# Optimization experiments

Hardware: AMD Instinct MI355X
Metric: run time of the kernel (lower is better)

## Reference

```python
import jax, jax.numpy as jnp
import numpy as np

N_NODES = 50000
N_EDGES = 800000
D = 64


def setup_inputs() -> dict:
    key = jax.random.key(0)
    k1, k2, k3, k4, k5, k6, k7 = jax.random.split(key, 7)
    h = jax.random.normal(k1, (N_NODES, D), dtype=jnp.float32)
    x = jax.random.normal(k2, (N_NODES, 3), dtype=jnp.float32)
    edge_index = jax.random.randint(k3, (2, N_EDGES), 0, N_NODES, dtype=jnp.int64)
    # fc_h: Linear(D, D); fc_x: Linear(D, 1). PyTorch default init scale ~1/sqrt(fan_in).
    s = 1.0 / np.sqrt(D)
    W_h = jax.random.uniform(k4, (D, D), minval=-s, maxval=s, dtype=jnp.float32)
    b_h = jax.random.uniform(k5, (D,), minval=-s, maxval=s, dtype=jnp.float32)
    W_x = jax.random.uniform(k6, (D, 1), minval=-s, maxval=s, dtype=jnp.float32)
    b_x = jax.random.uniform(k7, (1,), minval=-s, maxval=s, dtype=jnp.float32)
    return {"h": h, "x": x, "edge_index": edge_index,
            "W_h": W_h, "b_h": b_h, "W_x": W_x, "b_x": b_x}


def reference(h, x, edge_index, W_h, b_h, W_x, b_x):
    row, col = edge_index[0], edge_index[1]
    h_j = h[col]                                   # [E, D] gather
    delta_x = x[row] - x[col]                      # [E, 3]
    m = jax.nn.relu(h_j @ W_h + b_h)               # [E, D]
    agg_h = jax.ops.segment_sum(m, row, num_segments=h.shape[0])
    h_new = h + agg_h
    weight = jax.nn.relu(h_j @ W_x + b_x)          # [E, 1]
    agg_x = jax.ops.segment_sum(delta_x * weight, row, num_segments=x.shape[0])
    x_new = x + agg_x
    return (h_new, x_new)
```

## Files before the change

kernel.cpp:

```cpp
#include <hip/hip_runtime.h>
#include <hip/hip_fp16.h>

#define N_NODES 50000
#define N_EDGES 800000
#define D 64
#define BLOCK 256

#define NBIN 256
#define BINW 196
#define BCAP 3584
#define EPB 4096
#define NBINBLK 196
#define PREBLK 196
#define SUBS 4
#define RNODES 49
#define QCAP 1024

__global__ __launch_bounds__(BLOCK) void pre_bin_kernel(
    const float* __restrict__ h, const float* __restrict__ x,
    const int* __restrict__ eidx,
    const float* __restrict__ Wh, const float* __restrict__ bh,
    const float* __restrict__ Wx, const float* __restrict__ bx,
    __half2* __restrict__ M16, float4* __restrict__ px,
    int* __restrict__ bins, int* __restrict__ gcur) {
  const unsigned b = blockIdx.x;

  if (b < NBINBLK) {
    __shared__ int cnt[NBIN], ssc[NBIN], start[NBIN], cur[NBIN], gbase[NBIN];
    __shared__ int stage[EPB];
    const int t = threadIdx.x;
    cnt[t] = 0;
    __syncthreads();
    const int base = (int)b * EPB;
#pragma unroll 4
    for (int k = 0; k < EPB / BLOCK; ++k) {
      int e = base + k * BLOCK + t;
      if (e < N_EDGES) {
        int row = eidx[e];
        if ((unsigned)row < N_NODES) atomicAdd(&cnt[row / BINW], 1);
      }
    }
    __syncthreads();
    ssc[t] = cnt[t];
    __syncthreads();
    for (int off = 1; off < NBIN; off <<= 1) {
      int v = (t >= off) ? ssc[t - off] : 0;
      __syncthreads();
      ssc[t] += v;
      __syncthreads();
    }
    int ex = ssc[t] - cnt[t];
    start[t] = ex;
    cur[t] = ex;
    gbase[t] = cnt[t] ? atomicAdd(&gcur[t], cnt[t]) : 0;
    __syncthreads();
#pragma unroll 4
    for (int k = 0; k < EPB / BLOCK; ++k) {
      int e = base + k * BLOCK + t;
      if (e < N_EDGES) {
        int row = eidx[e];
        int col = eidx[N_EDGES + e];
        if ((unsigned)row < N_NODES && (unsigned)col < N_NODES) {
          int bb = row / BINW;
          int pos = atomicAdd(&cur[bb], 1);
          stage[pos] = (bb << 24) | ((row - bb * BINW) << 16) | col;
        }
      }
    }
    __syncthreads();
    const int total = ssc[NBIN - 1];
    for (int idx = t; idx < total; idx += BLOCK) {
      int e = stage[idx];
      int bb = ((unsigned)e) >> 24;
      int dst = gbase[bb] + (idx - start[bb]);
      if (dst < BCAP) bins[(size_t)bb * BCAP + dst] = e;
    }
    return;
  }

  const int pid = (int)b - NBINBLK;
  const int i = pid * BLOCK + threadIdx.x;
  if (i >= N_NODES) return;

  const float4* __restrict__ h4 = (const float4*)(h + (size_t)i * D);
  const float4* __restrict__ Wx4 = (const float4*)Wx;

  float acc[D];
#pragma unroll
  for (int d = 0; d < D; ++d) acc[d] = bh[d];
  float wx = bx[0];

  for (int q = 0; q < D / 4; ++q) {
    float4 hv = h4[q];
    float4 wxv = Wx4[q];
    wx = fmaf(hv.x, wxv.x, fmaf(hv.y, wxv.y, fmaf(hv.z, wxv.z,
         fmaf(hv.w, wxv.w, wx))));
#pragma unroll
    for (int r = 0; r < 4; ++r) {
      float hk = (r == 0) ? hv.x : (r == 1) ? hv.y : (r == 2) ? hv.z : hv.w;
      const float4* wr4 = (const float4*)(Wh + (q * 4 + r) * D);
#pragma unroll
      for (int dq = 0; dq < D / 4; ++dq) {
        float4 wv = wr4[dq];
        acc[4 * dq + 0] = fmaf(hk, wv.x, acc[4 * dq + 0]);
        acc[4 * dq + 1] = fmaf(hk, wv.y, acc[4 * dq + 1]);
        acc[4 * dq + 2] = fmaf(hk, wv.z, acc[4 * dq + 2]);
        acc[4 * dq + 3] = fmaf(hk, wv.w, acc[4 * dq + 3]);
      }
    }
  }

  __half2 hh[D / 2];
#pragma unroll
  for (int j = 0; j < D / 2; ++j)
    hh[j] = __floats2half2_rn(fmaxf(acc[2 * j], 0.0f),
                              fmaxf(acc[2 * j + 1], 0.0f));
  float4* mrow = (float4*)(M16 + (size_t)i * 32);
  const float4* hhp = (const float4*)hh;
#pragma unroll
  for (int q = 0; q < 8; ++q) mrow[q] = hhp[q];

  float w = fmaxf(wx, 0.0f);
  px[i] = make_float4(w, w * x[(size_t)i * 3 + 0],
                      w * x[(size_t)i * 3 + 1],
                      w * x[(size_t)i * 3 + 2]);
}

__global__ __launch_bounds__(256) void agg_kernel(
    const float* __restrict__ h, const float* __restrict__ x,
    const int* __restrict__ bins, const int* __restrict__ gcur,
    const __half2* __restrict__ M16, const float4* __restrict__ px,
    float* __restrict__ out) {
  __shared__ int qs[QCAP];
  __shared__ int hist[RNODES];
  __shared__ int rstart[RNODES + 1];
  __shared__ int rcur[RNODES];

  const int t = threadIdx.x;
  const int bin = blockIdx.x >> 2, sub = blockIdx.x & 3;
  const int lbase = sub * RNODES;
  const int gb = bin * BINW + lbase;
  const int R = min(RNODES, N_NODES - gb);
  if (R <= 0) return;

  if (t < RNODES) hist[t] = 0;
  __syncthreads();

  const int n = min(gcur[bin], BCAP);
  const int* bs = bins + (size_t)bin * BCAP;
  for (int i = t; i < n; i += 256) {
    int e = bs[i];
    unsigned dd = (unsigned)((e >> 16) & 0xff) - (unsigned)lbase;
    if (dd < (unsigned)R) atomicAdd(&hist[dd], 1);
  }
  __syncthreads();
  if (t < 64) {
    int myh = (t < R) ? hist[t] : 0;
    int v = myh;
#pragma unroll
    for (int off = 1; off < 64; off <<= 1) {
      int u = __shfl_up(v, off);
      if (t >= off) v += u;
    }
    if (t == 0) rstart[0] = 0;
    if (t < R) { rstart[t + 1] = v; rcur[t] = v - myh; }
  }
  __syncthreads();
  for (int i = t; i < n; i += 256) {
    int e = bs[i];
    unsigned dd = (unsigned)((e >> 16) & 0xff) - (unsigned)lbase;
    if (dd < (unsigned)R) {
      int pos = atomicAdd(&rcur[dd], 1);
      if (pos < QCAP) qs[pos] = e;
    }
  }
  __syncthreads();

  const float* pxf = (const float*)px;
  const float2* M2 = (const float2*)M16;
  const int l16 = t & 15;
  const int stream = t >> 4;
  const int wbase = t & 48;
  const size_t xb = (size_t)N_NODES * D;

  for (int rr = stream; rr < R; rr += 16) {
    int beg = min(rstart[rr], QCAP);
    int end = min(rstart[rr + 1], QCAP);
    float a0 = 0.f, a1 = 0.f, a2 = 0.f, a3 = 0.f, ps = 0.f;
    for (int qi = beg; qi < end; qi += 8) {
      float2 g[8];
      float pv[8];
      bool val[8];
#pragma unroll
      for (int j = 0; j < 8; ++j) {
        int idx = qi + j;
        val[j] = idx < end;
        int e = qs[val[j] ? idx : beg];
        int c = e & 0xffff;
        pv[j] = 0.f;
        if (val[j]) {
          g[j] = M2[(size_t)c * 16 + l16];
          if (l16 < 4) pv[j] = pxf[c * 4 + l16];
        }
      }
#pragma unroll
      for (int j = 0; j < 8; ++j)
        if (val[j]) {
          const __half2* hp = (const __half2*)&g[j];
          float2 f0 = __half22float2(hp[0]);
          float2 f1 = __half22float2(hp[1]);
          a0 += f0.x; a1 += f0.y; a2 += f1.x; a3 += f1.y;
          ps += pv[j];
        }
    }
    int gn = gb + rr;
    float4 hvv = ((const float4*)h)[(size_t)gn * 16 + l16];
    ((float4*)out)[(size_t)gn * 16 + l16] =
        make_float4(hvv.x + a0, hvv.y + a1, hvv.z + a2, hvv.w + a3);
    float W = __shfl(ps, wbase);
    float pc = __shfl(ps, wbase + l16 + 1);
    if (l16 < 3)
      out[xb + (size_t)gn * 3 + l16] =
          fmaf(x[(size_t)gn * 3 + l16], 1.0f + W, -pc);
  }
}


__global__ __launch_bounds__(256) void init_out_kernel(
    const float* __restrict__ h, const float* __restrict__ x,
    float* __restrict__ out) {
  const int NH4 = N_NODES * D / 4;
  const int NT4 = (N_NODES * D + N_NODES * 3) / 4;
  int i = blockIdx.x * 256 + threadIdx.x;
  if (i >= NT4) return;
  float4 v;
  if (i < NH4) v = ((const float4*)h)[i];
  else         v = ((const float4*)x)[i - NH4];
  ((float4*)out)[i] = v;
}

__global__ __launch_bounds__(256) void edge_kernel(
    const float* __restrict__ h, const float* __restrict__ x,
    const int* __restrict__ eidx,
    const float* __restrict__ Wh, const float* __restrict__ bh,
    const float* __restrict__ Wx, const float* __restrict__ bx,
    float* __restrict__ out) {
  int e = blockIdx.x * 256 + threadIdx.x;
  if (e >= N_EDGES) return;
  int row = eidx[e];
  int col = eidx[N_EDGES + e];
  if ((unsigned)row >= N_NODES || (unsigned)col >= N_NODES) return;
  const float* hj = h + (size_t)col * D;
  float acc[D];
#pragma unroll
  for (int dd = 0; dd < D; ++dd) acc[dd] = bh[dd];
  float wsum = bx[0];
#pragma unroll 2
  for (int kg = 0; kg < D / 4; ++kg) {
    float4 hv = *(const float4*)(hj + kg * 4);
#pragma unroll
    for (int j = 0; j < 4; ++j) {
      float hk = (j == 0) ? hv.x : (j == 1) ? hv.y : (j == 2) ? hv.z : hv.w;
      int k = kg * 4 + j;
      wsum = fmaf(hk, Wx[k], wsum);
      const float* wrow = Wh + k * D;
#pragma unroll
      for (int dd = 0; dd < D; ++dd) acc[dd] = fmaf(hk, wrow[dd], acc[dd]);
    }
  }
  float* outh = out + (size_t)row * D;
#pragma unroll
  for (int dd = 0; dd < D; ++dd) atomicAdd(&outh[dd], fmaxf(acc[dd], 0.0f));
  float w = fmaxf(wsum, 0.0f);
  float* outx = out + (size_t)N_NODES * D + (size_t)row * 3;
  const float* xr = x + (size_t)row * 3;
  const float* xc = x + (size_t)col * 3;
#pragma unroll
  for (int c = 0; c < 3; ++c) atomicAdd(&outx[c], (xr[c] - xc[c]) * w);
}


extern "C" void kernel_launch(void* const* d_in, const int* in_sizes, int n_in,
                              void* d_out, int out_size, void* d_ws, size_t ws_size,
                              hipStream_t stream) {
  const float* h    = (const float*)d_in[0];
  const float* x    = (const float*)d_in[1];
  const int*   eidx = (const int*)d_in[2];
  const float* Wh   = (const float*)d_in[3];
  const float* bh   = (const float*)d_in[4];
  const float* Wx   = (const float*)d_in[5];
  const float* bx   = (const float*)d_in[6];
  float* out = (float*)d_out;

  size_t need = (size_t)N_NODES * D * 2 + (size_t)N_NODES * 16 +
                (size_t)NBIN * BCAP * 4 + 1024;

  if (ws_size < need) {
    const int NT4 = (N_NODES * D + N_NODES * 3) / 4;
    init_out_kernel<<<(NT4 + 255) / 256, 256, 0, stream>>>(h, x, out);
    edge_kernel<<<(N_EDGES + 255) / 256, 256, 0, stream>>>(
        h, x, eidx, Wh, bh, Wx, bx, out);
    return;
  }

  __half2* M16 = (__half2*)d_ws;
  float4*  px  = (float4*)((char*)d_ws + (size_t)N_NODES * D * 2);
  int*     bins = (int*)((char*)px + (size_t)N_NODES * 16);
  int*     gcur = bins + (size_t)NBIN * BCAP;

  hipMemsetAsync(gcur, 0, NBIN * sizeof(int), stream);
  pre_bin_kernel<<<NBINBLK + PREBLK, BLOCK, 0, stream>>>(
      h, x, eidx, Wh, bh, Wx, bx, M16, px, bins, gcur);
  agg_kernel<<<NBIN * SUBS, 256, 0, stream>>>(
      h, x, bins, gcur, M16, px, out);
}
```

Measured before the change: 128.6 us.

## Fuse binning, node transform and aggregation into one cooperative kernel

Merges the pre-bin/node-transform kernel and the aggregation kernel into a single cooperative launch of 512 blocks separated by a grid-wide sync. Each block both bins a slice of edges and computes M16/px for 98 nodes, then aggregates half a bin, staging the bin's entries in LDS before the two passes. The aim is to remove one kernel launch boundary and spread work over more blocks. The cost is a grid barrier, larger LDS use that may limit residency, and only 98 of 256 threads doing the dense node transform, with the old two-kernel path kept as a fallback if the cooperative launch fails.

```diff
diff --git a/kernel.cpp b/kernel.cpp
--- a/kernel.cpp
+++ b/kernel.cpp
@@ -1,20 +1,247 @@
 #include <hip/hip_runtime.h>
 #include <hip/hip_fp16.h>
+#include <hip/hip_cooperative_groups.h>
+
+namespace cg = cooperative_groups;
 
 #define N_NODES 50000
 #define N_EDGES 800000
 #define D 64
 #define BLOCK 256
+#define GRID 512
 
 #define NBIN 256
 #define BINW 196
 #define BCAP 3584
+#define EPBF 1563
+#define KITF 7
+#define STAGEB 1568
+#define RNODES 98
+#define QCAP 1920
+
 #define EPB 4096
 #define NBINBLK 196
 #define PREBLK 196
-#define SUBS 4
-#define RNODES 49
-#define QCAP 1024
+#define SUBS_F 4
+#define RN_F 49
+#define QCAP_F 1024
+
+__global__ __launch_bounds__(BLOCK) void fused_kernel(
+    const float* __restrict__ h, const float* __restrict__ x,
+    const int* __restrict__ eidx,
+    const float* __restrict__ Wh, const float* __restrict__ bh,
+    const float* __restrict__ Wx, const float* __restrict__ bx,
+    __half2* __restrict__ M16, float4* __restrict__ px,
+    int* __restrict__ bins, int* __restrict__ gcur,
+    float* __restrict__ out) {
+  __shared__ union {
+    struct {
+      int cnt[NBIN], ssc[NBIN], start[NBIN], cur[NBIN], gbase[NBIN];
+      int stage[STAGEB];
+    } bl;
+    struct {
+      int stage2[BCAP];
+      int qs[QCAP];
+      int sc[128];
+      int hist[RNODES], rcur[RNODES];
+      int rstart[RNODES + 1];
+    } ag;
+  } S;
+
+  const int b = blockIdx.x;
+  const int t = threadIdx.x;
+
+  S.bl.cnt[t] = 0;
+  __syncthreads();
+  const int ebase = b * EPBF;
+  const int eend = min(ebase + EPBF, N_EDGES);
+#pragma unroll
+  for (int k = 0; k < KITF; ++k) {
+    int e = ebase + k * BLOCK + t;
+    if (e < eend) {
+      int row = eidx[e];
+      if ((unsigned)row < N_NODES) atomicAdd(&S.bl.cnt[row / BINW], 1);
+    }
+  }
+  __syncthreads();
+  S.bl.ssc[t] = S.bl.cnt[t];
+  __syncthreads();
+  for (int off = 1; off < NBIN; off <<= 1) {
+    int v = (t >= off) ? S.bl.ssc[t - off] : 0;
+    __syncthreads();
+    S.bl.ssc[t] += v;
+    __syncthreads();
+  }
+  {
+    int ex = S.bl.ssc[t] - S.bl.cnt[t];
+    S.bl.start[t] = ex;
+    S.bl.cur[t] = ex;
+    S.bl.gbase[t] = S.bl.cnt[t] ? atomicAdd(&gcur[t], S.bl.cnt[t]) : 0;
+  }
+  __syncthreads();
+#pragma unroll
+  for (int k = 0; k < KITF; ++k) {
+    int e = ebase + k * BLOCK + t;
+    if (e < eend) {
+      int row = eidx[e];
+      int col = eidx[N_EDGES + e];
+      if ((unsigned)row < N_NODES && (unsigned)col < N_NODES) {
+        int bb = row / BINW;
+        int pos = atomicAdd(&S.bl.cur[bb], 1);
+        S.bl.stage[pos] = (bb << 24) | ((row - bb * BINW) << 16) | col;
+      }
+    }
+  }
+  __syncthreads();
+  {
+    const int total = S.bl.ssc[NBIN - 1];
+    for (int idx = t; idx < total; idx += BLOCK) {
+      int e = S.bl.stage[idx];
+      int bb = ((unsigned)e) >> 24;
+      int dst = S.bl.gbase[bb] + (idx - S.bl.start[bb]);
+      if (dst < BCAP) bins[(size_t)bb * BCAP + dst] = e;
+    }
+  }
+
+  {
+    const int i = b * RNODES + t;
+    if (t < RNODES && i < N_NODES) {
+      const float4* __restrict__ h4 = (const float4*)(h + (size_t)i * D);
+      const float4* __restrict__ Wx4 = (const float4*)Wx;
+      float acc[D];
+#pragma unroll
+      for (int d = 0; d < D; ++d) acc[d] = bh[d];
+      float wx = bx[0];
+      for (int q = 0; q < D / 4; ++q) {
+        float4 hv = h4[q];
+        float4 wxv = Wx4[q];
+        wx = fmaf(hv.x, wxv.x, fmaf(hv.y, wxv.y,
+             fmaf(hv.z, wxv.z, fmaf(hv.w, wxv.w, wx))));
+#pragma unroll
+        for (int r = 0; r < 4; ++r) {
+          float hk = (r == 0) ? hv.x : (r == 1) ? hv.y : (r == 2) ? hv.z : hv.w;
+          const float4* wr4 = (const float4*)(Wh + (q * 4 + r) * D);
+#pragma unroll
+          for (int dq = 0; dq < D / 4; ++dq) {
+            float4 wv = wr4[dq];
+            acc[4 * dq + 0] = fmaf(hk, wv.x, acc[4 * dq + 0]);
+            acc[4 * dq + 1] = fmaf(hk, wv.y, acc[4 * dq + 1]);
+            acc[4 * dq + 2] = fmaf(hk, wv.z, acc[4 * dq + 2]);
+            acc[4 * dq + 3] = fmaf(hk, wv.w, acc[4 * dq + 3]);
+          }
+        }
+      }
+      __half2 hh[D / 2];
+#pragma unroll
+      for (int j = 0; j < D / 2; ++j)
+        hh[j] = __floats2half2_rn(fmaxf(acc[2 * j], 0.0f),
+                                  fmaxf(acc[2 * j + 1], 0.0f));
+      float4* mrow = (float4*)(M16 + (size_t)i * 32);
+      const float4* hhp = (const float4*)hh;
+#pragma unroll
+      for (int q = 0; q < 8; ++q) mrow[q] = hhp[q];
+      float w = fmaxf(wx, 0.0f);
+      px[i] = make_float4(w, w * x[(size_t)i * 3 + 0],
+                          w * x[(size_t)i * 3 + 1],
+                          w * x[(size_t)i * 3 + 2]);
+    }
+  }
+
+  __threadfence();
+  cg::this_grid().sync();
+  __threadfence();
+
+  {
+    const int bin = b >> 1, sub = b & 1;
+    const int lbase = sub * RNODES;
+    const int gb = bin * BINW + lbase;
+    const int R = min(RNODES, N_NODES - gb);
+    if (R > 0) {
+      if (t < RNODES) S.ag.hist[t] = 0;
+      __syncthreads();
+      const int n = min(gcur[bin], BCAP);
+      const int* bs = bins + (size_t)bin * BCAP;
+      for (int ii = t; ii < n; ii += BLOCK) {
+        int e = bs[ii];
+        S.ag.stage2[ii] = e;
+        unsigned dd = (unsigned)((e >> 16) & 0xff) - (unsigned)lbase;
+        if (dd < (unsigned)R) atomicAdd(&S.ag.hist[dd], 1);
+      }
+      __syncthreads();
+      if (t < 128) S.ag.sc[t] = (t < R) ? S.ag.hist[t] : 0;
+      __syncthreads();
+      for (int off = 1; off < 128; off <<= 1) {
+        int v = (t < 128 && t >= off) ? S.ag.sc[t - off] : 0;
+        __syncthreads();
+        if (t < 128) S.ag.sc[t] += v;
+        __syncthreads();
+      }
+      if (t == 0) S.ag.rstart[0] = 0;
+      if (t < R) {
+        S.ag.rstart[t + 1] = S.ag.sc[t];
+        S.ag.rcur[t] = S.ag.sc[t] - S.ag.hist[t];
+      }
+      __syncthreads();
+      for (int ii = t; ii < n; ii += BLOCK) {
+        int e = S.ag.stage2[ii];
+        unsigned dd = (unsigned)((e >> 16) & 0xff) - (unsigned)lbase;
+        if (dd < (unsigned)R) {
+          int pos = atomicAdd(&S.ag.rcur[dd], 1);
+          if (pos < QCAP) S.ag.qs[pos] = e;
+        }
+      }
+      __syncthreads();
+
+      const float* pxf = (const float*)px;
+      const float2* M2 = (const float2*)M16;
+      const int l16 = t & 15;
+      const int stream = t >> 4;
+      const int wbase = t & 48;
+      const size_t xb = (size_t)N_NODES * D;
+
+      for (int rr = stream; rr < R; rr += 16) {
+        int beg = min(S.ag.rstart[rr], QCAP);
+        int end = min(S.ag.rstart[rr + 1], QCAP);
+        float a0 = 0.f, a1 = 0.f, a2 = 0.f, a3 = 0.f, ps = 0.f;
+        for (int qi = beg; qi < end; qi += 8) {
+          float2 g[8];
+          float pv[8];
+          bool val[8];
+#pragma unroll
+          for (int j = 0; j < 8; ++j) {
+            int idx = qi + j;
+            val[j] = idx < end;
+            int e = S.ag.qs[val[j] ? idx : beg];
+            int c = e & 0xffff;
+            pv[j] = 0.f;
+            if (val[j]) {
+              g[j] = M2[(size_t)c * 16 + l16];
+              if (l16 < 4) pv[j] = pxf[c * 4 + l16];
+            }
+          }
+#pragma unroll
+          for (int j = 0; j < 8; ++j)
+            if (val[j]) {
+              const __half2* hp = (const __half2*)&g[j];
+              float2 f0 = __half22float2(hp[0]);
+              float2 f1 = __half22float2(hp[1]);
+              a0 += f0.x; a1 += f0.y; a2 += f1.x; a3 += f1.y;
+              ps += pv[j];
+            }
+        }
+        int gn = gb + rr;
+        float4 hvv = ((const float4*)h)[(size_t)gn * 16 + l16];
+        ((float4*)out)[(size_t)gn * 16 + l16] =
+            make_float4(hvv.x + a0, hvv.y + a1, hvv.z + a2, hvv.w + a3);
+        float W = __shfl(ps, wbase);
+        float pc = __shfl(ps, wbase + l16 + 1);
+        if (l16 < 3)
+          out[xb + (size_t)gn * 3 + l16] =
+              fmaf(x[(size_t)gn * 3 + l16], 1.0f + W, -pc);
+      }
+    }
+  }
+}
 
 __global__ __launch_bounds__(BLOCK) void pre_bin_kernel(
     const float* __restrict__ h, const float* __restrict__ x,
@@ -24,7 +251,6 @@
     __half2* __restrict__ M16, float4* __restrict__ px,
     int* __restrict__ bins, int* __restrict__ gcur) {
   const unsigned b = blockIdx.x;
-
   if (b < NBINBLK) {
     __shared__ int cnt[NBIN], ssc[NBIN], start[NBIN], cur[NBIN], gbase[NBIN];
     __shared__ int stage[EPB];
@@ -50,8 +276,7 @@
       __syncthreads();
     }
     int ex = ssc[t] - cnt[t];
-    start[t] = ex;
-    cur[t] = ex;
+    start[t] = ex; cur[t] = ex;
     gbase[t] = cnt[t] ? atomicAdd(&gcur[t], cnt[t]) : 0;
     __syncthreads();
 #pragma unroll 4
@@ -77,19 +302,15 @@
     }
     return;
   }
-
   const int pid = (int)b - NBINBLK;
   const int i = pid * BLOCK + threadIdx.x;
   if (i >= N_NODES) return;
-
   const float4* __restrict__ h4 = (const float4*)(h + (size_t)i * D);
   const float4* __restrict__ Wx4 = (const float4*)Wx;
-
   float acc[D];
 #pragma unroll
   for (int d = 0; d < D; ++d) acc[d] = bh[d];
   float wx = bx[0];
-
   for (int q = 0; q < D / 4; ++q) {
     float4 hv = h4[q];
     float4 wxv = Wx4[q];
@@ -109,7 +330,6 @@
       }
     }
   }
-
   __half2 hh[D / 2];
 #pragma unroll
   for (int j = 0; j < D / 2; ++j)
@@ -119,11 +339,9 @@
   const float4* hhp = (const float4*)hh;
 #pragma unroll
   for (int q = 0; q < 8; ++q) mrow[q] = hhp[q];
-
   float w = fmaxf(wx, 0.0f);
   px[i] = make_float4(w, w * x[(size_t)i * 3 + 0],
-                      w * x[(size_t)i * 3 + 1],
-                      w * x[(size_t)i * 3 + 2]);
+                      w * x[(size_t)i * 3 + 1], w * x[(size_t)i * 3 + 2]);
 }
 
 __global__ __launch_bounds__(256) void agg_kernel(
@@ -131,21 +349,16 @@
     const int* __restrict__ bins, const int* __restrict__ gcur,
     const __half2* __restrict__ M16, const float4* __restrict__ px,
     float* __restrict__ out) {
-  __shared__ int qs[QCAP];
-  __shared__ int hist[RNODES];
-  __shared__ int rstart[RNODES + 1];
-  __shared__ int rcur[RNODES];
-
+  __shared__ int qs[QCAP_F];
+  __shared__ int hist[RN_F], rstart[RN_F + 1], rcur[RN_F];
   const int t = threadIdx.x;
   const int bin = blockIdx.x >> 2, sub = blockIdx.x & 3;
-  const int lbase = sub * RNODES;
+  const int lbase = sub * RN_F;
   const int gb = bin * BINW + lbase;
-  const int R = min(RNODES, N_NODES - gb);
+  const int R = min(RN_F, N_NODES - gb);
   if (R <= 0) return;
-
-  if (t < RNODES) hist[t] = 0;
-  __syncthreads();
-
+  if (t < RN_F) hist[t] = 0;
+  __syncthreads();
   const int n = min(gcur[bin], BCAP);
   const int* bs = bins + (size_t)bin * BCAP;
   for (int i = t; i < n; i += 256) {
@@ -171,26 +384,22 @@
     unsigned dd = (unsigned)((e >> 16) & 0xff) - (unsigned)lbase;
     if (dd < (unsigned)R) {
       int pos = atomicAdd(&rcur[dd], 1);
-      if (pos < QCAP) qs[pos] = e;
-    }
-  }
-  __syncthreads();
-
+      if (pos < QCAP_F) qs[pos] = e;
+    }
+  }
+  __syncthreads();
   const float* pxf = (const float*)px;
   const float2* M2 = (const float2*)M16;
   const int l16 = t & 15;
   const int stream = t >> 4;
   const int wbase = t & 48;
   const size_t xb = (size_t)N_NODES * D;
-
   for (int rr = stream; rr < R; rr += 16) {
-    int beg = min(rstart[rr], QCAP);
-    int end = min(rstart[rr + 1], QCAP);
+    int beg = min(rstart[rr], QCAP_F);
+    int end = min(rstart[rr + 1], QCAP_F);
     float a0 = 0.f, a1 = 0.f, a2 = 0.f, a3 = 0.f, ps = 0.f;
     for (int qi = beg; qi < end; qi += 8) {
-      float2 g[8];
-      float pv[8];
-      bool val[8];
+      float2 g[8]; float pv[8]; bool val[8];
 #pragma unroll
       for (int j = 0; j < 8; ++j) {
         int idx = qi + j;
@@ -224,7 +433,6 @@
           fmaf(x[(size_t)gn * 3 + l16], 1.0f + W, -pc);
   }
 }
-
 
 __global__ __launch_bounds__(256) void init_out_kernel(
     const float* __restrict__ h, const float* __restrict__ x,
@@ -279,7 +487,6 @@
   for (int c = 0; c < 3; ++c) atomicAdd(&outx[c], (xr[c] - xc[c]) * w);
 }
 
-
 extern "C" void kernel_launch(void* const* d_in, const int* in_sizes, int n_in,
                               void* d_out, int out_size, void* d_ws, size_t ws_size,
                               hipStream_t stream) {
@@ -309,8 +516,17 @@
   int*     gcur = bins + (size_t)NBIN * BCAP;
 
   hipMemsetAsync(gcur, 0, NBIN * sizeof(int), stream);
-  pre_bin_kernel<<<NBINBLK + PREBLK, BLOCK, 0, stream>>>(
-      h, x, eidx, Wh, bh, Wx, bx, M16, px, bins, gcur);
-  agg_kernel<<<NBIN * SUBS, 256, 0, stream>>>(
-      h, x, bins, gcur, M16, px, out);
+
+  void* kargs[] = {(void*)&h, (void*)&x, (void*)&eidx, (void*)&Wh,
+                   (void*)&bh, (void*)&Wx, (void*)&bx, (void*)&M16,
+                   (void*)&px, (void*)&bins, (void*)&gcur, (void*)&out};
+  hipError_t rc = hipLaunchCooperativeKernel(
+      reinterpret_cast<void*>(fused_kernel), dim3(GRID), dim3(BLOCK),
+      kargs, 0, stream);
+  if (rc != hipSuccess) {
+    pre_bin_kernel<<<NBINBLK + PREBLK, BLOCK, 0, stream>>>(
+        h, x, eidx, Wh, bh, Wx, bx, M16, px, bins, gcur);
+    agg_kernel<<<NBIN * SUBS_F, 256, 0, stream>>>(
+        h, x, bins, gcur, M16, px, out);
+  }
 }
```

Measured after the change: 306.5 us. +138.5%, slower.

## Split aggregation by source-node half and stage bin edges in LDS

Applied to the files above, without the earlier changes.

The aggregation kernel now sorts each destination's edges into two buckets by whether the source node falls in the lower or upper half of node indices. Each thread stream processes all its rows for one half before moving to the other, which aims to keep the gathered message rows in a smaller working set for cache locality. Bin entries are staged in shared memory so the second pass reads LDS instead of global memory. The binning kernel also uses twice as many blocks with half the edges each, which adds more blocks and more global atomics to raise parallelism.

```diff
diff --git a/kernel.cpp b/kernel.cpp
--- a/kernel.cpp
+++ b/kernel.cpp
@@ -9,12 +9,15 @@
 #define NBIN 256
 #define BINW 196
 #define BCAP 3584
-#define EPB 4096
-#define NBINBLK 196
+#define EPB 2048
+#define KIT 8
+#define NBINBLK 391
 #define PREBLK 196
 #define SUBS 4
 #define RNODES 49
 #define QCAP 1024
+#define HALF_COL 25000
+#define ROWS_PS 4
 
 __global__ __launch_bounds__(BLOCK) void pre_bin_kernel(
     const float* __restrict__ h, const float* __restrict__ x,
@@ -32,8 +35,8 @@
     cnt[t] = 0;
     __syncthreads();
     const int base = (int)b * EPB;
-#pragma unroll 4
-    for (int k = 0; k < EPB / BLOCK; ++k) {
+#pragma unroll
+    for (int k = 0; k < KIT; ++k) {
       int e = base + k * BLOCK + t;
       if (e < N_EDGES) {
         int row = eidx[e];
@@ -54,8 +57,8 @@
     cur[t] = ex;
     gbase[t] = cnt[t] ? atomicAdd(&gcur[t], cnt[t]) : 0;
     __syncthreads();
-#pragma unroll 4
-    for (int k = 0; k < EPB / BLOCK; ++k) {
+#pragma unroll
+    for (int k = 0; k < KIT; ++k) {
       int e = base + k * BLOCK + t;
       if (e < N_EDGES) {
         int row = eidx[e];
@@ -131,10 +134,11 @@
     const int* __restrict__ bins, const int* __restrict__ gcur,
     const __half2* __restrict__ M16, const float4* __restrict__ px,
     float* __restrict__ out) {
+  __shared__ int stage2[BCAP];
   __shared__ int qs[QCAP];
-  __shared__ int hist[RNODES];
-  __shared__ int rstart[RNODES + 1];
-  __shared__ int rcur[RNODES];
+  __shared__ int sc[128];
+  __shared__ int hist[2 * RNODES], rcur[2 * RNODES];
+  __shared__ int rstart[2 * RNODES + 1];
 
   const int t = threadIdx.x;
   const int bin = blockIdx.x >> 2, sub = blockIdx.x & 3;
@@ -143,34 +147,41 @@
   const int R = min(RNODES, N_NODES - gb);
   if (R <= 0) return;
 
-  if (t < RNODES) hist[t] = 0;
+  if (t < 2 * RNODES) hist[t] = 0;
   __syncthreads();
 
   const int n = min(gcur[bin], BCAP);
   const int* bs = bins + (size_t)bin * BCAP;
   for (int i = t; i < n; i += 256) {
     int e = bs[i];
-    unsigned dd = (unsigned)((e >> 16) & 0xff) - (unsigned)lbase;
-    if (dd < (unsigned)R) atomicAdd(&hist[dd], 1);
-  }
-  __syncthreads();
-  if (t < 64) {
-    int myh = (t < R) ? hist[t] : 0;
-    int v = myh;
-#pragma unroll
-    for (int off = 1; off < 64; off <<= 1) {
-      int u = __shfl_up(v, off);
-      if (t >= off) v += u;
-    }
-    if (t == 0) rstart[0] = 0;
-    if (t < R) { rstart[t + 1] = v; rcur[t] = v - myh; }
-  }
-  __syncthreads();
-  for (int i = t; i < n; i += 256) {
-    int e = bs[i];
+    stage2[i] = e;
     unsigned dd = (unsigned)((e >> 16) & 0xff) - (unsigned)lbase;
     if (dd < (unsigned)R) {
-      int pos = atomicAdd(&rcur[dd], 1);
+      int kk = (int)dd * 2 + ((e & 0xffff) >= HALF_COL);
+      atomicAdd(&hist[kk], 1);
+    }
+  }
+  __syncthreads();
+  if (t < 128) sc[t] = (t < 2 * R) ? hist[t] : 0;
+  __syncthreads();
+  for (int off = 1; off < 128; off <<= 1) {
+    int v = (t < 128 && t >= off) ? sc[t - off] : 0;
+    __syncthreads();
+    if (t < 128) sc[t] += v;
+    __syncthreads();
+  }
+  if (t == 0) rstart[0] = 0;
+  if (t < 2 * R) {
+    rstart[t + 1] = sc[t];
+    rcur[t] = sc[t] - hist[t];
+  }
+  __syncthreads();
+  for (int i = t; i < n; i += 256) {
+    int e = stage2[i];
+    unsigned dd = (unsigned)((e >> 16) & 0xff) - (unsigned)lbase;
+    if (dd < (unsigned)R) {
+      int kk = (int)dd * 2 + ((e & 0xffff) >= HALF_COL);
+      int pos = atomicAdd(&rcur[kk], 1);
       if (pos < QCAP) qs[pos] = e;
     }
   }
@@ -183,45 +194,67 @@
   const int wbase = t & 48;
   const size_t xb = (size_t)N_NODES * D;
 
-  for (int rr = stream; rr < R; rr += 16) {
-    int beg = min(rstart[rr], QCAP);
-    int end = min(rstart[rr + 1], QCAP);
-    float a0 = 0.f, a1 = 0.f, a2 = 0.f, a3 = 0.f, ps = 0.f;
-    for (int qi = beg; qi < end; qi += 8) {
-      float2 g[8];
-      float pv[8];
-      bool val[8];
-#pragma unroll
-      for (int j = 0; j < 8; ++j) {
-        int idx = qi + j;
-        val[j] = idx < end;
-        int e = qs[val[j] ? idx : beg];
-        int c = e & 0xffff;
-        pv[j] = 0.f;
-        if (val[j]) {
-          g[j] = M2[(size_t)c * 16 + l16];
-          if (l16 < 4) pv[j] = pxf[c * 4 + l16];
+  float ac[ROWS_PS][4];
+  float ps[ROWS_PS];
+#pragma unroll
+  for (int k = 0; k < ROWS_PS; ++k) {
+    ac[k][0] = ac[k][1] = ac[k][2] = ac[k][3] = 0.f;
+    ps[k] = 0.f;
+  }
+
+  for (int hf = 0; hf < 2; ++hf) {
+#pragma unroll
+    for (int k = 0; k < ROWS_PS; ++k) {
+      int rr = stream + 16 * k;
+      if (rr < R) {
+        int beg = min(rstart[2 * rr + hf], QCAP);
+        int end = min(rstart[2 * rr + hf + 1], QCAP);
+        for (int qi = beg; qi < end; qi += 8) {
+          float2 g[8];
+          float pv[8];
+          bool val[8];
+#pragma unroll
+          for (int j = 0; j < 8; ++j) {
+            int idx = qi + j;
+            val[j] = idx < end;
+            int e = qs[val[j] ? idx : beg];
+            int c = e & 0xffff;
+            pv[j] = 0.f;
+            if (val[j]) {
+              g[j] = M2[(size_t)c * 16 + l16];
+              if (l16 < 4) pv[j] = pxf[c * 4 + l16];
+            }
+          }
+#pragma unroll
+          for (int j = 0; j < 8; ++j)
+            if (val[j]) {
+              const __half2* hp = (const __half2*)&g[j];
+              float2 f0 = __half22float2(hp[0]);
+              float2 f1 = __half22float2(hp[1]);
+              ac[k][0] += f0.x; ac[k][1] += f0.y;
+              ac[k][2] += f1.x; ac[k][3] += f1.y;
+              ps[k] += pv[j];
+            }
         }
       }
-#pragma unroll
-      for (int j = 0; j < 8; ++j)
-        if (val[j]) {
-          const __half2* hp = (const __half2*)&g[j];
-          float2 f0 = __half22float2(hp[0]);
-          float2 f1 = __half22float2(hp[1]);
-          a0 += f0.x; a1 += f0.y; a2 += f1.x; a3 += f1.y;
-          ps += pv[j];
-        }
-    }
-    int gn = gb + rr;
-    float4 hvv = ((const float4*)h)[(size_t)gn * 16 + l16];
-    ((float4*)out)[(size_t)gn * 16 + l16] =
-        make_float4(hvv.x + a0, hvv.y + a1, hvv.z + a2, hvv.w + a3);
-    float W = __shfl(ps, wbase);
-    float pc = __shfl(ps, wbase + l16 + 1);
-    if (l16 < 3)
-      out[xb + (size_t)gn * 3 + l16] =
-          fmaf(x[(size_t)gn * 3 + l16], 1.0f + W, -pc);
+    }
+  }
+
+#pragma unroll
+  for (int k = 0; k < ROWS_PS; ++k) {
+    int rr = stream + 16 * k;
+    if (rr < R) {
+      int gn = gb + rr;
+      float4 hvv = ((const float4*)h)[(size_t)gn * 16 + l16];
+      ((float4*)out)[(size_t)gn * 16 + l16] =
+          make_float4(hvv.x + ac[k][0], hvv.y + ac[k][1],
+                      hvv.z + ac[k][2], hvv.w + ac[k][3]);
+      float W = __shfl(ps[k], wbase);
+      float pc = __shfl(ps[k], wbase + l16 + 1);
+      if (l16 < 3)
+        out[xb + (size_t)gn * 3 + l16] =
+            fmaf(x[(size_t)gn * 3 + l16], 1.0f + W, -pc);
+    }
   }
 }
 
```

Result: slower. 140.3 us (+9.1%).

## Split aggregation into finer sub-bins and stage bin edges in LDS

Applied to the files above, without the earlier changes.

The aggregation kernel now gives each bin eight blocks of 25 destination nodes instead of four blocks of 49, which doubles the block count and raises parallelism. The bin's edge list is copied into shared memory on the first pass so the second pass reads it from LDS rather than global memory. Each 16-lane stream now handles at most two rows with fixed-size accumulators and separates the px loads from the M loads. The trade-off is that every block still scans the whole bin, so redundant scanning doubles, and the extra LDS use may limit occupancy.

```diff
diff --git a/kernel.cpp b/kernel.cpp
--- a/kernel.cpp
+++ b/kernel.cpp
@@ -12,9 +12,10 @@
 #define EPB 4096
 #define NBINBLK 196
 #define PREBLK 196
-#define SUBS 4
-#define RNODES 49
-#define QCAP 1024
+#define SUBS 8
+#define RNODES 25
+#define QCAP 576
+#define ROWS_PS 2
 
 __global__ __launch_bounds__(BLOCK) void pre_bin_kernel(
     const float* __restrict__ h, const float* __restrict__ x,
@@ -126,21 +127,21 @@
                       w * x[(size_t)i * 3 + 2]);
 }
 
-__global__ __launch_bounds__(256) void agg_kernel(
+__global__ __launch_bounds__(256, 8) void agg_kernel(
     const float* __restrict__ h, const float* __restrict__ x,
     const int* __restrict__ bins, const int* __restrict__ gcur,
     const __half2* __restrict__ M16, const float4* __restrict__ px,
     float* __restrict__ out) {
+  __shared__ int stage2[BCAP];
   __shared__ int qs[QCAP];
-  __shared__ int hist[RNODES];
+  __shared__ int hist[RNODES], rcur[RNODES];
   __shared__ int rstart[RNODES + 1];
-  __shared__ int rcur[RNODES];
 
   const int t = threadIdx.x;
-  const int bin = blockIdx.x >> 2, sub = blockIdx.x & 3;
+  const int bin = blockIdx.x >> 3, sub = blockIdx.x & 7;
   const int lbase = sub * RNODES;
   const int gb = bin * BINW + lbase;
-  const int R = min(RNODES, N_NODES - gb);
+  const int R = min(min(RNODES, BINW - lbase), N_NODES - gb);
   if (R <= 0) return;
 
   if (t < RNODES) hist[t] = 0;
@@ -150,6 +151,7 @@
   const int* bs = bins + (size_t)bin * BCAP;
   for (int i = t; i < n; i += 256) {
     int e = bs[i];
+    stage2[i] = e;
     unsigned dd = (unsigned)((e >> 16) & 0xff) - (unsigned)lbase;
     if (dd < (unsigned)R) atomicAdd(&hist[dd], 1);
   }
@@ -167,7 +169,7 @@
   }
   __syncthreads();
   for (int i = t; i < n; i += 256) {
-    int e = bs[i];
+    int e = stage2[i];
     unsigned dd = (unsigned)((e >> 16) & 0xff) - (unsigned)lbase;
     if (dd < (unsigned)R) {
       int pos = atomicAdd(&rcur[dd], 1);
@@ -183,45 +185,67 @@
   const int wbase = t & 48;
   const size_t xb = (size_t)N_NODES * D;
 
-  for (int rr = stream; rr < R; rr += 16) {
-    int beg = min(rstart[rr], QCAP);
-    int end = min(rstart[rr + 1], QCAP);
-    float a0 = 0.f, a1 = 0.f, a2 = 0.f, a3 = 0.f, ps = 0.f;
-    for (int qi = beg; qi < end; qi += 8) {
-      float2 g[8];
-      float pv[8];
-      bool val[8];
-#pragma unroll
-      for (int j = 0; j < 8; ++j) {
-        int idx = qi + j;
-        val[j] = idx < end;
-        int e = qs[val[j] ? idx : beg];
-        int c = e & 0xffff;
-        pv[j] = 0.f;
-        if (val[j]) {
-          g[j] = M2[(size_t)c * 16 + l16];
-          if (l16 < 4) pv[j] = pxf[c * 4 + l16];
+  float ac[ROWS_PS][4];
+  float ps[ROWS_PS];
+#pragma unroll
+  for (int k = 0; k < ROWS_PS; ++k) {
+    ac[k][0] = ac[k][1] = ac[k][2] = ac[k][3] = 0.f;
+    ps[k] = 0.f;
+  }
+
+#pragma unroll
+  for (int k = 0; k < ROWS_PS; ++k) {
+    int rr = stream + 16 * k;
+    if (rr < R) {
+      int beg = min(rstart[rr], QCAP);
+      int end = min(rstart[rr + 1], QCAP);
+      for (int qi = beg; qi < end; qi += 8) {
+        float2 g[8];
+        float pv[8];
+        bool val[8];
+        int cs[8];
+#pragma unroll
+        for (int j = 0; j < 8; ++j) {
+          int idx = qi + j;
+          val[j] = idx < end;
+          int e = qs[val[j] ? idx : beg];
+          cs[j] = e & 0xffff;
+          if (val[j]) g[j] = M2[(size_t)cs[j] * 16 + l16];
         }
+#pragma unroll
+        for (int j = 0; j < 8; ++j) {
+          pv[j] = 0.f;
+          if (val[j] && l16 < 4) pv[j] = pxf[cs[j] * 4 + l16];
+        }
+#pragma unroll
+        for (int j = 0; j < 8; ++j)
+          if (val[j]) {
+            const __half2* hp = (const __half2*)&g[j];
+            float2 f0 = __half22float2(hp[0]);
+            float2 f1 = __half22float2(hp[1]);
+            ac[k][0] += f0.x; ac[k][1] += f0.y;
+            ac[k][2] += f1.x; ac[k][3] += f1.y;
+            ps[k] += pv[j];
+          }
       }
-#pragma unroll
-      for (int j = 0; j < 8; ++j)
-        if (val[j]) {
-          const __half2* hp = (const __half2*)&g[j];
-          float2 f0 = __half22float2(hp[0]);
-          float2 f1 = __half22float2(hp[1]);
-          a0 += f0.x; a1 += f0.y; a2 += f1.x; a3 += f1.y;
-          ps += pv[j];
-        }
-    }
-    int gn = gb + rr;
-    float4 hvv = ((const float4*)h)[(size_t)gn * 16 + l16];
-    ((float4*)out)[(size_t)gn * 16 + l16] =
-        make_float4(hvv.x + a0, hvv.y + a1, hvv.z + a2, hvv.w + a3);
-    float W = __shfl(ps, wbase);
-    float pc = __shfl(ps, wbase + l16 + 1);
-    if (l16 < 3)
-      out[xb + (size_t)gn * 3 + l16] =
-          fmaf(x[(size_t)gn * 3 + l16], 1.0f + W, -pc);
+    }
+  }
+
+#pragma unroll
+  for (int k = 0; k < ROWS_PS; ++k) {
+    int rr = stream + 16 * k;
+    if (rr < R) {
+      int gn = gb + rr;
+      float4 hvv = ((const float4*)h)[(size_t)gn * 16 + l16];
+      ((float4*)out)[(size_t)gn * 16 + l16] =
+          make_float4(hvv.x + ac[k][0], hvv.y + ac[k][1],
+                      hvv.z + ac[k][2], hvv.w + ac[k][3]);
+      float W = __shfl(ps[k], wbase);
+      float pc = __shfl(ps[k], wbase + l16 + 1);
+      if (l16 < 3)
+        out[xb + (size_t)gn * 3 + l16] =
+            fmaf(x[(size_t)gn * 3 + l16], 1.0f + W, -pc);
+    }
   }
 }
 
```

Measured after the change: 127.9 us. Within noise of the previous version (-0.5%).
